# Optimization experiments

Hardware: AMD Instinct MI355X
Metric: run time of the kernel (lower is better)

## Reference

```python
import jax, jax.numpy as jnp
import numpy as np
from jax import lax

B, LS, LT, C, H, GRID = 32, 256, 128, 768, 12, 16
KEEP_RATIO = 0.7

def _ln(x, w, b):
    mu = x.mean(-1, keepdims=True)
    var = ((x - mu) ** 2).mean(-1, keepdims=True)
    return (x - mu) / jnp.sqrt(var + 1e-5) * w + b

def _gelu(x):
    return jax.nn.gelu(x, approximate=False)

def setup_inputs() -> dict:
    key = jax.random.key(0)
    ks = jax.random.split(key, 16)
    w = lambda k, s: jax.random.normal(k, s, jnp.float32) * 0.02
    N = LT + LS
    return {
        'x': jax.random.normal(ks[0], (B, N, C), jnp.float32),
        'global_index_template': jax.random.randint(ks[1], (B, LT), 0, LT).astype(jnp.int32),
        'global_index_search': jax.random.randint(ks[2], (B, LS), 0, LS).astype(jnp.int32),
        'learn_template_mask': jax.random.uniform(ks[3], (2, B, LT // 2), jnp.float32),
        'ln1_w': jnp.ones((C,), jnp.float32), 'ln1_b': jnp.zeros((C,), jnp.float32),
        'qkv_w': w(ks[4], (C, 3 * C)),
        'proj_w': w(ks[5], (C, C)), 'proj_b': jnp.zeros((C,), jnp.float32),
        'ln2_w': jnp.ones((C,), jnp.float32), 'ln2_b': jnp.zeros((C,), jnp.float32),
        'fc1_w': w(ks[6], (C, 4 * C)), 'fc1_b': jnp.zeros((4 * C,), jnp.float32),
        'fc2_w': w(ks[7], (4 * C, C)), 'fc2_b': jnp.zeros((C,), jnp.float32),
        'd1_w': w(ks[8], (3 * C, 768)), 'd1_b': jnp.zeros((768,), jnp.float32),
        'd2_w': w(ks[9], (768, 384)), 'd2_b': jnp.zeros((384,), jnp.float32),
        'd3_w': w(ks[10], (384, 192)), 'd3_b': jnp.zeros((192,), jnp.float32),
        'd4_w': w(ks[11], (192, 1)), 'd4_b': jnp.zeros((1,), jnp.float32),
    }

def reference(x, global_index_template, global_index_search, learn_template_mask,
              ln1_w, ln1_b, qkv_w, proj_w, proj_b, ln2_w, ln2_b,
              fc1_w, fc1_b, fc2_w, fc2_b,
              d1_w, d1_b, d2_w, d2_b, d3_w, d3_b, d4_w, d4_b):
    bs = x.shape[0]
    lt = global_index_template.shape[1]
    ls = global_index_search.shape[1]
    half = lt // 2
    # --- roimax target representations ---
    init_rep = jnp.max(x[:, :half] * learn_template_mask[0][..., None], axis=1, keepdims=True)   # [B,1,C]
    dyn_rep = jnp.max(x[:, half:lt] * learn_template_mask[1][..., None], axis=1, keepdims=True)  # [B,1,C]
    feat = jnp.concatenate([x[:, -ls:],
                            jnp.broadcast_to(init_rep, (bs, ls, C)),
                            jnp.broadcast_to(dyn_rep, (bs, ls, C))], axis=-1)  # [B,ls,3C]
    h = _gelu(feat @ d1_w + d1_b)
    h = _gelu(h @ d2_w + d2_b)
    h = _gelu(h @ d3_w + d3_b)
    pred = h @ d4_w + d4_b                      # [B,ls,1]
    probs = jax.nn.sigmoid(pred)                # foreground probabilities
    # --- 3x3 region-sum conv and argmax center ---
    grid = probs.reshape(bs, 1, GRID, GRID)
    kern = jnp.ones((1, 1, 3, 3), grid.dtype)
    filt = lax.conv_general_dilated(grid, kern, (1, 1), 'SAME',
                                    dimension_numbers=('NCHW', 'OIHW', 'NCHW'))
    max_idx = jnp.argmax(filt.reshape(bs, -1), axis=1)
    cx, cy = max_idx // GRID, max_idx % GRID
    gx = jnp.arange(GRID)[None, :, None]
    gy = jnp.arange(GRID)[None, None, :]
    win = lambda r: ((jnp.abs(gx - cx[:, None, None]) <= r) &
                     (jnp.abs(gy - cy[:, None, None]) <= r)).reshape(bs, GRID * GRID)
    mask7, mask11 = win(3), win(5)
    foreground = (probs > 0.5).astype(jnp.int32)          # [B,ls,1]
    selected_fg = foreground * mask7[..., None].astype(jnp.int32)
    # --- candidate elimination: keep all tokens inside 11x11 window first, then top prob ---
    lens_keep = int(np.ceil(KEEP_RATIO * ls))
    p_out = jnp.where(mask11, jnp.inf, probs[..., 0])     # [B,ls]
    order = jnp.argsort(-p_out, axis=1)                   # stable descending
    topk_idx, non_topk = order[:, :lens_keep], order[:, lens_keep:]
    keep_index = jnp.take_along_axis(global_index_search, topk_idx, axis=1)
    removed_index = jnp.take_along_axis(global_index_search, non_topk, axis=1)
    xs = jnp.take_along_axis(x[:, lt:], topk_idx[..., None], axis=1)  # [B,lens_keep,C]
    xnew = jnp.concatenate([x[:, :lt], xs], axis=1)       # [B, lt+lens_keep, C]
    sf = jnp.take_along_axis(selected_fg, topk_idx[..., None], axis=1)[..., 0]
    decision = jax.nn.one_hot(sf, 2, dtype=x.dtype)       # scatter_(2, sf, 1)
    search_policy = jnp.concatenate([jnp.zeros((bs, lens_keep, 2), x.dtype), decision], -1)
    template_policy = jnp.zeros((bs, half, 4), x.dtype).at[:, :, 0].set(1.0)
    dynamic_policy = jnp.zeros((bs, half, 4), x.dtype).at[:, :, 1].set(1.0)
    P = jnp.concatenate([template_policy, dynamic_policy, search_policy], axis=1)
    key_bg = P[:, :, 2] > 0.5    # background search tokens -> masked as attention keys
    # --- attention ---
    n = xnew.shape[1]
    dh = C // H
    hn = _ln(xnew, ln1_w, ln1_b)
    qkv = (hn @ qkv_w).reshape(bs, n, 3, H, dh).transpose(2, 0, 3, 1, 4)
    q, k, v = qkv[0], qkv[1], qkv[2]
    scores = jnp.einsum('bhnd,bhmd->bhnm', q, k) * dh ** -0.5
    scores = jnp.where(key_bg[:, None, None, :], -1e9, scores)
    attn = jax.nn.softmax(scores, axis=-1)
    out = jnp.einsum('bhnm,bhmd->bhnd', attn, v).transpose(0, 2, 1, 3).reshape(bs, n, C)
    xnew = xnew + (out @ proj_w + proj_b)
    m = _ln(xnew, ln2_w, ln2_b)
    xout = xnew + (_gelu(m @ fc1_w + fc1_b) @ fc2_w + fc2_b)
    return (xout, keep_index, removed_index, attn)
```

## Files before the change

kernel.cpp:

```cpp
#include <hip/hip_runtime.h>
#include <hip/hip_bf16.h>
#include <math.h>

#define BB 32
#define LSN 256
#define LTN 128
#define CCH 768
#define NHH 12
#define NTOK 384
#define NKEEP 180
#define NREM 76
#define NNEW 308
#define MS 8192
#define MN 9856

typedef unsigned short u16;
typedef __attribute__((ext_vector_type(8))) short s8v;
typedef __attribute__((ext_vector_type(4))) float f4v;

__device__ __forceinline__ u16 f2bf(float x) {
    union { __hip_bfloat16 b; u16 u; } c; c.b = __float2bfloat16(x); return c.u;
}
__device__ __forceinline__ float bf2f(u16 u) {
    return __uint_as_float(((unsigned)u) << 16);
}
__device__ __forceinline__ void gl_lds16(const u16* g, u16* l) {
    __builtin_amdgcn_global_load_lds((const __attribute__((address_space(1))) unsigned*)g,
                                     (__attribute__((address_space(3))) unsigned*)l, 16, 0, 0);
}

__global__ void k_fail(float* o, float v) { o[0] = v; }

__global__ void k_reps(const float* __restrict__ x, const float* __restrict__ mask,
                       float* __restrict__ rep0, float* __restrict__ rep1) {
    int b = blockIdx.x, t = threadIdx.x;
    for (int c = t; c < CCH; c += 256) {
        float m0 = -INFINITY, m1 = -INFINITY;
        for (int i = 0; i < 64; ++i) {
            float v0 = x[(size_t)(b * NTOK + i) * CCH + c] * mask[b * 64 + i];
            float v1 = x[(size_t)(b * NTOK + 64 + i) * CCH + c] * mask[BB * 64 + b * 64 + i];
            m0 = fmaxf(m0, v0); m1 = fmaxf(m1, v1);
        }
        rep0[b * CCH + c] = m0; rep1[b * CCH + c] = m1;
    }
}

__device__ __forceinline__ float gelu_np(float v) {
    float t = v / 1.4142135623730951f;
    float ef = (float)erf((double)t);
    return 0.5f * v * (1.0f + ef);
}

template<int ROWMAP>
__global__ __launch_bounds__(256) void gemm_exact(const float* __restrict__ A,
                                                  const float* __restrict__ rep0, const float* __restrict__ rep1,
                                                  const float* __restrict__ W, const float* __restrict__ bias,
                                                  float* __restrict__ out, int N, int K) {
    __shared__ float As[32 * 64];
    __shared__ float Bs[32 * 64];
    int t = threadIdx.x;
    int tx = t & 15, ty = t >> 4;
    int bm = blockIdx.y * 64, bn = blockIdx.x * 64;
    int b = bm >> 8;
    float acc[4][4] = {};

    int arow = t >> 2;
    int ak = (t & 3) * 4;
    int asw = arow ^ ((ak & 4) << 2);
    size_t aoff;
    if (ROWMAP) aoff = (size_t)(b * NTOK + LTN + ((bm + arow) & 255)) * CCH;
    else        aoff = (size_t)(bm + arow) * K;

    int bkr = t >> 4, bc = (t & 15) * 4;

#define LOADA(kg) (ROWMAP ? (((kg) < CCH) ? *(const float4*)&A[aoff + (kg)] \
                    : (((kg) < 2*CCH) ? *(const float4*)&rep0[b*CCH + (kg) - CCH] \
                                      : *(const float4*)&rep1[b*CCH + (kg) - 2*CCH])) \
                   : *(const float4*)&A[aoff + (kg)])

    int nt = K >> 5;
    float4 ra0 = LOADA(ak), ra1 = LOADA(16 + ak);
    float4 rb0 = *(const float4*)&W[(size_t)bkr * N + bn + bc];
    float4 rb1 = *(const float4*)&W[(size_t)(16 + bkr) * N + bn + bc];

    for (int tile = 0; tile < nt; ++tile) {
        __syncthreads();
        As[(ak + 0) * 64 + asw] = ra0.x; As[(ak + 1) * 64 + asw] = ra0.y;
        As[(ak + 2) * 64 + asw] = ra0.z; As[(ak + 3) * 64 + asw] = ra0.w;
        As[(16 + ak + 0) * 64 + asw] = ra1.x; As[(16 + ak + 1) * 64 + asw] = ra1.y;
        As[(16 + ak + 2) * 64 + asw] = ra1.z; As[(16 + ak + 3) * 64 + asw] = ra1.w;
        *(float4*)&Bs[t * 4] = rb0;
        *(float4*)&Bs[1024 + t * 4] = rb1;
        if (tile + 1 < nt) {
            int k0 = (tile + 1) << 5;
            ra0 = LOADA(k0 + ak); ra1 = LOADA(k0 + 16 + ak);
            rb0 = *(const float4*)&W[(size_t)(k0 + bkr) * N + bn + bc];
            rb1 = *(const float4*)&W[(size_t)(k0 + 16 + bkr) * N + bn + bc];
        }
        __syncthreads();
#pragma unroll
        for (int k = 0; k < 32; ++k) {
            float a[4], bv[4];
            *(float4*)&a[0]  = *(const float4*)&As[k * 64 + ((ty * 4) ^ ((k & 4) << 2))];
            *(float4*)&bv[0] = *(const float4*)&Bs[k * 64 + tx * 4];
#pragma unroll
            for (int i = 0; i < 4; ++i)
#pragma unroll
                for (int j = 0; j < 4; ++j) acc[i][j] = fmaf(a[i], bv[j], acc[i][j]);
        }
    }
#undef LOADA
#pragma unroll
    for (int i = 0; i < 4; ++i) {
        int m = bm + ty * 4 + i;
        float4 o;
        o.x = gelu_np(acc[i][0] + bias[bn + tx * 4 + 0]);
        o.y = gelu_np(acc[i][1] + bias[bn + tx * 4 + 1]);
        o.z = gelu_np(acc[i][2] + bias[bn + tx * 4 + 2]);
        o.w = gelu_np(acc[i][3] + bias[bn + tx * 4 + 3]);
        *(float4*)&out[(size_t)m * N + bn + tx * 4] = o;
    }
}

__global__ void k_d4(const float* __restrict__ h3, const float* __restrict__ w4,
                     const float* __restrict__ b4, float* __restrict__ probs) {
    int m = blockIdx.x * 256 + threadIdx.x;
    if (m >= MS) return;
    float acc = 0.f;
    for (int k = 0; k < 192; ++k) acc = fmaf(h3[(size_t)m * 192 + k], w4[k], acc);
    float pred = acc + b4[0];
    float ef = (float)exp(-(double)pred);
    probs[m] = 1.0f / (1.0f + ef);
}

__global__ void k_select(const float* __restrict__ probs, float* __restrict__ pout, int* __restrict__ sf) {
    int b = blockIdx.x, t = threadIdx.x;
    __shared__ float pr[256];
    __shared__ double ft[256];
    __shared__ int cxy[2];
    pr[t] = probs[b * 256 + t];
    __syncthreads();
    int X = t >> 4, Y = t & 15;
    double s = 0.0;
    for (int dx = -1; dx <= 1; ++dx)
        for (int dy = -1; dy <= 1; ++dy) {
            int xx = X + dx, yy = Y + dy;
            if (xx >= 0 && xx < 16 && yy >= 0 && yy < 16) s += (double)pr[xx * 16 + yy];
        }
    ft[t] = s;
    __syncthreads();
    if (t == 0) {
        double best = ft[0]; int bi = 0;
        for (int i = 1; i < 256; ++i) if (ft[i] > best) { best = ft[i]; bi = i; }
        cxy[0] = bi >> 4; cxy[1] = bi & 15;
    }
    __syncthreads();
    int cx = cxy[0], cy = cxy[1];
    int ax = X - cx; if (ax < 0) ax = -ax;
    int ay = Y - cy; if (ay < 0) ay = -ay;
    bool m7  = (ax <= 3) && (ay <= 3);
    bool m11 = (ax <= 5) && (ay <= 5);
    int fg = (pr[t] > 0.5f) ? 1 : 0;
    sf[b * 256 + t] = m7 ? fg : 0;
    pout[b * 256 + t] = m11 ? INFINITY : pr[t];
}

__global__ void k_sort(const float* __restrict__ pout, const int* __restrict__ sf, const int* __restrict__ gis,
                       float* __restrict__ keep_out, float* __restrict__ rem_out,
                       int* __restrict__ topk, int* __restrict__ keybg) {
    int b = blockIdx.x, t = threadIdx.x;
    __shared__ float p[256];
    __shared__ int ord[256];
    p[t] = pout[b * 256 + t];
    __syncthreads();
    float pi = p[t];
    int rank = 0;
    for (int j = 0; j < 256; ++j) {
        float pj = p[j];
        rank += (pj > pi) || (pj == pi && j < t);
    }
    ord[rank] = t;
    __syncthreads();
    int idx = ord[t];
    int g = gis[b * 256 + idx];
    if (t < NKEEP) {
        keep_out[b * NKEEP + t] = (float)g;
        topk[b * NKEEP + t] = idx;
        keybg[b * NNEW + LTN + t] = (sf[b * 256 + idx] == 0) ? 1 : 0;
    } else {
        rem_out[b * NREM + (t - NKEEP)] = (float)g;
    }
    if (t < LTN) keybg[b * NNEW + t] = 0;
}

__global__ void k_xnew(const float* __restrict__ x, const int* __restrict__ topk, float* __restrict__ xn) {
    int row = blockIdx.x;
    int b = row / NNEW, r = row - b * NNEW;
    int src = (r < LTN) ? r : (LTN + topk[b * NKEEP + (r - LTN)]);
    const float* s = x + (size_t)(b * NTOK + src) * CCH;
    float* d = xn + (size_t)row * CCH;
    for (int c = threadIdx.x; c < CCH; c += 256) d[c] = s[c];
}


__global__ void k_ln_bf(const float* __restrict__ in, const float* __restrict__ w, const float* __restrict__ b,
                        u16* __restrict__ out) {
    int row = blockIdx.x, t = threadIdx.x;
    __shared__ float s1[256], s2[256];
    const float* p = in + (size_t)row * CCH;
    float v[3]; float a0 = 0.f, a1 = 0.f;
#pragma unroll
    for (int i = 0; i < 3; ++i) { v[i] = p[t + 256 * i]; a0 += v[i]; a1 += v[i] * v[i]; }
    s1[t] = a0; s2[t] = a1;
    __syncthreads();
    for (int off = 128; off > 0; off >>= 1) {
        if (t < off) { s1[t] += s1[t + off]; s2[t] += s2[t + off]; }
        __syncthreads();
    }
    float mu = s1[0] * (1.0f / CCH);
    float var = s2[0] * (1.0f / CCH) - mu * mu;
    float rstd = rsqrtf(var + 1e-5f);
#pragma unroll
    for (int i = 0; i < 3; ++i) {
        int c = t + 256 * i;
        out[(size_t)row * CCH + c] = f2bf((v[i] - mu) * rstd * w[c] + b[c]);
    }
}

__global__ void k_wT(const float* __restrict__ W, u16* __restrict__ Wt, int K, int N) {
    __shared__ float tile[32][33];
    int k0 = blockIdx.x * 32, n0 = blockIdx.y * 32;
    int tx = threadIdx.x, ty = threadIdx.y;
    for (int i = ty; i < 32; i += 8) tile[i][tx] = W[(size_t)(k0 + i) * N + n0 + tx];
    __syncthreads();
    for (int i = ty; i < 32; i += 8) Wt[(size_t)(n0 + i) * K + k0 + tx] = f2bf(tile[tx][i]);
}

template<int MODE>
__global__ __launch_bounds__(256) void gemm_bf16(const u16* __restrict__ A, const u16* __restrict__ Bt,
                                                 const float* __restrict__ bias, const float* __restrict__ res,
                                                 float* __restrict__ outf, u16* __restrict__ outb,
                                                 u16* __restrict__ vT, int N, int K) {
    __shared__ u16 sm[2][2][4096];
    int t = threadIdx.x, lane = t & 63, wid = t >> 6;
    int bm = blockIdx.y * 128, bn = blockIdx.x * 128;
    const u16* pA[2]; const u16* pB[2];
#pragma unroll
    for (int i = 0; i < 2; ++i) {
        int L = wid * 128 + i * 64 + lane;
        int line = L >> 3, sp = L & 7, sl = sp ^ (line & 7);
        int r = (line << 1) | (sl >> 2), k0 = (sl & 3) << 3;
        pA[i] = A + (size_t)(bm + r) * K + k0;
        pB[i] = Bt + (size_t)(bn + r) * K + k0;
    }
    int wr = wid >> 1, wc = wid & 1;
    int l15 = lane & 15, l4 = lane >> 4;
    int rA = wr * 64 + l15, rB = wc * 64 + l15;
    int offA = (rA >> 1) * 128 + (((((rA & 1) << 2) | l4)) ^ ((rA >> 1) & 7)) * 16;
    int offB = (rB >> 1) * 128 + (((((rB & 1) << 2) | l4)) ^ ((rB >> 1) & 7)) * 16;
    f4v zero = {0.f, 0.f, 0.f, 0.f};
    f4v acc[4][4];
#pragma unroll
    for (int i = 0; i < 4; ++i)
#pragma unroll
        for (int j = 0; j < 4; ++j) acc[i][j] = zero;

#define STAGE_G(buf, kt) { \
    u16* da = &sm[buf][0][wid * 1024]; u16* db = &sm[buf][1][wid * 1024]; \
    gl_lds16(pA[0] + (kt) * 32, da); \
    gl_lds16(pA[1] + (kt) * 32, da + 512); \
    gl_lds16(pB[0] + (kt) * 32, db); \
    gl_lds16(pB[1] + (kt) * 32, db + 512); \
}
    int nk = K >> 5;
    STAGE_G(0, 0);
    __syncthreads();
    for (int kt = 0; kt < nk; ++kt) {
        int cur = kt & 1;
        if (kt + 1 < nk) STAGE_G(cur ^ 1, kt + 1);
        const char* bA = (const char*)&sm[cur][0][0];
        const char* bBp = (const char*)&sm[cur][1][0];
        s8v a[4], b[4];
#pragma unroll
        for (int i = 0; i < 4; ++i) {
            a[i] = *(const s8v*)(bA + offA + i * 1024);
            b[i] = *(const s8v*)(bBp + offB + i * 1024);
        }
#pragma unroll
        for (int mf = 0; mf < 4; ++mf)
#pragma unroll
            for (int nf = 0; nf < 4; ++nf)
                acc[mf][nf] = __builtin_amdgcn_mfma_f32_16x16x32_bf16(a[mf], b[nf], acc[mf][nf], 0, 0, 0);
        __syncthreads();
    }
#undef STAGE_G
#pragma unroll
    for (int mf = 0; mf < 4; ++mf)
#pragma unroll
        for (int nf = 0; nf < 4; ++nf)
#pragma unroll
            for (int j = 0; j < 4; ++j) {
                int row = bm + wr * 64 + mf * 16 + l4 * 4 + j;
                int col = bn + wc * 64 + nf * 16 + l15;
                float v = acc[mf][nf][j];
                if (MODE == 0) {
                    if (col < 1536) {
                        if (col < 768) v *= 0.125f;
                        outb[(size_t)row * 1536 + col] = f2bf(v);
                    } else {
                        int c2 = col - 1536, hh = c2 >> 6, dd = c2 & 63;
                        int bb = row / NNEW, tok = row - bb * NNEW;
                        vT[(((size_t)bb * NHH + hh) * 64 + dd) * 312 + tok] = f2bf(v);
                    }
                } else if (MODE == 1) {
                    outf[(size_t)row * N + col] = v + bias[col] + res[(size_t)row * N + col];
                } else {
                    float g = v + bias[col];
                    g = 0.5f * g * (1.0f + erff(g * 0.70710678f));
                    outb[(size_t)row * N + col] = f2bf(g);
                }
            }
}

__global__ __launch_bounds__(256) void k_attn2(const u16* __restrict__ qkvQK, const u16* __restrict__ vT,
                                               const int* __restrict__ keybg,
                                               float* __restrict__ attn_out, u16* __restrict__ ctx) {
    __shared__ __align__(16) char smem[98560];
    u16* Qs = (u16*)smem;
    u16* Ks = (u16*)(smem + 9216);
    u16* Ss = (u16*)(smem + 55296);
    int* kb = (int*)(smem + 97280);
    float* OT = (float*)Ss;
    u16* Vts = Ks;

    int bh = blockIdx.y; int b = bh / NHH, h = bh % NHH;
    int q0 = blockIdx.x * 64;
    int nq = NNEW - q0; if (nq > 64) nq = 64;
    int t = threadIdx.x, lane = t & 63, wid = t >> 6;
    int l15 = lane & 15, l4 = lane >> 4;
    s8v z = {0, 0, 0, 0, 0, 0, 0, 0};

    {
        int r = t >> 2, c = (t & 3) * 16;
        u16* dst = Qs + r * 72 + c;
        if (r < nq) {
            const u16* src = qkvQK + (size_t)(b * NNEW + q0 + r) * 1536 + h * 64 + c;
            *(s8v*)dst = *(const s8v*)src;
            *(s8v*)(dst + 8) = *(const s8v*)(src + 8);
        } else { *(s8v*)dst = z; *(s8v*)(dst + 8) = z; }
    }
    for (int it = 0; it < 5; ++it) {
        int r = it * 64 + (t >> 2), c = (t & 3) * 16;
        u16* dst = Ks + r * 72 + c;
        if (r < NNEW) {
            const u16* src = qkvQK + (size_t)(b * NNEW + r) * 1536 + 768 + h * 64 + c;
            *(s8v*)dst = *(const s8v*)src;
            *(s8v*)(dst + 8) = *(const s8v*)(src + 8);
        } else { *(s8v*)dst = z; *(s8v*)(dst + 8) = z; }
    }
    for (int i = t; i < 320; i += 256) kb[i] = (i < NNEW) ? keybg[b * NNEW + i] : 1;
    __syncthreads();

    f4v zero = {0.f, 0.f, 0.f, 0.f};
    f4v acc[4][5];
#pragma unroll
    for (int i = 0; i < 4; ++i)
#pragma unroll
        for (int j = 0; j < 5; ++j) acc[i][j] = zero;
#pragma unroll
    for (int ks = 0; ks < 2; ++ks) {
        s8v a[4], bf[5];
#pragma unroll
        for (int mf = 0; mf < 4; ++mf) a[mf] = *(const s8v*)(Qs + (mf * 16 + l15) * 72 + ks * 32 + l4 * 8);
#pragma unroll
        for (int nf = 0; nf < 5; ++nf) bf[nf] = *(const s8v*)(Ks + (wid * 80 + nf * 16 + l15) * 72 + ks * 32 + l4 * 8);
#pragma unroll
        for (int mf = 0; mf < 4; ++mf)
#pragma unroll
            for (int nf = 0; nf < 5; ++nf)
                acc[mf][nf] = __builtin_amdgcn_mfma_f32_16x16x32_bf16(a[mf], bf[nf], acc[mf][nf], 0, 0, 0);
    }
#pragma unroll
    for (int nf = 0; nf < 5; ++nf) {
        int n = wid * 80 + nf * 16 + l15;
        int msk = kb[n];
#pragma unroll
        for (int mf = 0; mf < 4; ++mf)
#pragma unroll
            for (int j = 0; j < 4; ++j) {
                int q = mf * 16 + l4 * 4 + j;
                float v = msk ? -1e9f : acc[mf][nf][j];
                Ss[q * 328 + n] = f2bf(v);
            }
    }
    __syncthreads();

    {
        int d = t >> 2;
        for (int c = (t & 3); c < 39; c += 4) {
            const u16* src = vT + ((size_t)bh * 64 + d) * 312 + c * 8;
            *(s8v*)(Vts + d * 312 + c * 8) = *(const s8v*)src;
        }
    }
    {
        int q = t >> 2, j4 = t & 3;
        u16* row = Ss + q * 328 + j4 * 80;
        float mx = -3e38f;
#pragma unroll
        for (int i = 0; i < 10; ++i) {
            s8v vv = *(const s8v*)(row + i * 8);
#pragma unroll
            for (int e = 0; e < 8; ++e) mx = fmaxf(mx, bf2f((u16)vv[e]));
        }
        mx = fmaxf(mx, __shfl_xor(mx, 1));
        mx = fmaxf(mx, __shfl_xor(mx, 2));
        float sum = 0.f;
#pragma unroll
        for (int i = 0; i < 10; ++i) {
            s8v vv = *(const s8v*)(row + i * 8);
            s8v ov;
#pragma unroll
            for (int e = 0; e < 8; ++e) {
                float ex = expf(bf2f((u16)vv[e]) - mx);
                sum += ex;
                ov[e] = (short)f2bf(ex);
            }
            *(s8v*)(row + i * 8) = ov;
        }
        sum += __shfl_xor(sum, 1);
        sum += __shfl_xor(sum, 2);
        float inv = 1.0f / sum;
#pragma unroll
        for (int i = 0; i < 10; ++i) {
            s8v vv = *(const s8v*)(row + i * 8);
            s8v ov;
            float pf[8];
#pragma unroll
            for (int e = 0; e < 8; ++e) {
                float p = bf2f((u16)vv[e]) * inv;
                pf[e] = p;
                ov[e] = (short)f2bf(p);
            }
            *(s8v*)(row + i * 8) = ov;
            if (q < nq) {
                int n0 = j4 * 80 + i * 8;
                float* dst = attn_out + ((size_t)bh * NNEW + q0 + q) * NNEW + n0;
#pragma unroll
                for (int e = 0; e < 8; ++e) if (n0 + e < NNEW) dst[e] = pf[e];
            }
        }
    }
    __syncthreads();

    f4v o[4];
#pragma unroll
    for (int i = 0; i < 4; ++i) o[i] = zero;
    int dblk = wid * 16;
#pragma unroll
    for (int ks = 0; ks < 10; ++ks) {
        s8v av = *(const s8v*)(Vts + (dblk + l15) * 312 + ks * 32 + l4 * 8);
#pragma unroll
        for (int nf = 0; nf < 4; ++nf) {
            s8v pv = *(const s8v*)(Ss + (nf * 16 + l15) * 328 + ks * 32 + l4 * 8);
            o[nf] = __builtin_amdgcn_mfma_f32_16x16x32_bf16(av, pv, o[nf], 0, 0, 0);
        }
    }
    __syncthreads();
#pragma unroll
    for (int nf = 0; nf < 4; ++nf)
#pragma unroll
        for (int j = 0; j < 4; ++j)
            OT[(dblk + l4 * 4 + j) * 65 + nf * 16 + l15] = o[nf][j];
    __syncthreads();
    {
        int q = t >> 2, c = t & 3;
        if (q < nq) {
            u16 buf[16];
#pragma unroll
            for (int i = 0; i < 16; ++i) buf[i] = f2bf(OT[(c * 16 + i) * 65 + q]);
            u16* dst = ctx + (size_t)(b * NNEW + q0 + q) * CCH + h * 64 + c * 16;
            *(s8v*)dst = *(const s8v*)&buf[0];
            *(s8v*)(dst + 8) = *(const s8v*)&buf[8];
        }
    }
}

extern "C" void kernel_launch(void* const* d_in, const int* in_sizes, int n_in,
                              void* d_out, int out_size, void* d_ws, size_t ws_size,
                              hipStream_t stream) {
    const float* x     = (const float*)d_in[0];
    const int*   gis   = (const int*)d_in[2];
    const float* mask  = (const float*)d_in[3];
    const float* ln1w  = (const float*)d_in[4];
    const float* ln1b  = (const float*)d_in[5];
    const float* qkvw  = (const float*)d_in[6];
    const float* projw = (const float*)d_in[7];
    const float* projb = (const float*)d_in[8];
    const float* ln2w  = (const float*)d_in[9];
    const float* ln2b  = (const float*)d_in[10];
    const float* fc1w  = (const float*)d_in[11];
    const float* fc1b  = (const float*)d_in[12];
    const float* fc2w  = (const float*)d_in[13];
    const float* fc2b  = (const float*)d_in[14];
    const float* d1w   = (const float*)d_in[15];
    const float* d1b   = (const float*)d_in[16];
    const float* d2w   = (const float*)d_in[17];
    const float* d2b   = (const float*)d_in[18];
    const float* d3w   = (const float*)d_in[19];
    const float* d3b   = (const float*)d_in[20];
    const float* d4w   = (const float*)d_in[21];
    const float* d4b   = (const float*)d_in[22];

    float* out_x    = (float*)d_out;
    float* out_keep = out_x + 7569408;
    float* out_rem  = out_keep + 5760;
    float* out_attn = out_rem + 2432;

    char* ws = (char*)d_ws;
    u16* hn_bf  = (u16*)(ws);
    u16* qkvQK  = (u16*)(ws + 15138816);
    u16* vTb    = (u16*)(ws + 45416448);
    u16* fc1_bf = (u16*)(ws);
    u16* ctx_bf = (u16*)(ws + 60751872);
    u16* qkvwT  = (u16*)(ws + 75890688);
    u16* projwT = (u16*)(ws + 79429632);
    u16* fc1wT  = (u16*)(ws + 80609280);
    u16* fc2wT  = (u16*)(ws + 85327872);
    char* misc  = ws + 90046464;
    float* rep0  = (float*)(misc + 0 * 262144);
    float* rep1  = (float*)(misc + 1 * 262144);
    float* probs = (float*)(misc + 2 * 262144);
    float* pout  = (float*)(misc + 3 * 262144);
    int*   sf    = (int*)(misc + 4 * 262144);
    int*   topk  = (int*)(misc + 5 * 262144);
    int*   keybg = (int*)(misc + 6 * 262144);
    size_t required = 90046464ull + 7ull * 262144ull;
    if (ws_size < required) {
        k_fail<<<1, 1, 0, stream>>>((float*)d_out, (float)(ws_size / 1048576.0));
        return;
    }

    float* h1 = (float*)out_attn;
    float* h2 = h1 + 8192 * 768;
    float* h3 = h2 + 8192 * 384;

    k_wT<<<dim3(24, 72), dim3(32, 8), 0, stream>>>(qkvw, qkvwT, 768, 2304);
    k_wT<<<dim3(24, 24), dim3(32, 8), 0, stream>>>(projw, projwT, 768, 768);
    k_wT<<<dim3(24, 96), dim3(32, 8), 0, stream>>>(fc1w, fc1wT, 768, 3072);
    k_wT<<<dim3(96, 24), dim3(32, 8), 0, stream>>>(fc2w, fc2wT, 3072, 768);
    hipMemsetAsync(vTb, 0, 15335424, stream);

    k_reps<<<BB, 256, 0, stream>>>(x, mask, rep0, rep1);
    gemm_exact<1><<<dim3(12, 128), 256, 0, stream>>>(x, rep0, rep1, d1w, d1b, h1, 768, 2304);
    gemm_exact<0><<<dim3(6, 128), 256, 0, stream>>>(h1, nullptr, nullptr, d2w, d2b, h2, 384, 768);
    gemm_exact<0><<<dim3(3, 128), 256, 0, stream>>>(h2, nullptr, nullptr, d3w, d3b, h3, 192, 384);
    k_d4<<<MS / 256, 256, 0, stream>>>(h3, d4w, d4b, probs);
    k_select<<<BB, 256, 0, stream>>>(probs, pout, sf);
    k_sort<<<BB, 256, 0, stream>>>(pout, sf, gis, out_keep, out_rem, topk, keybg);
    k_xnew<<<MN, 256, 0, stream>>>(x, topk, out_x);

    k_ln_bf<<<MN, 256, 0, stream>>>(out_x, ln1w, ln1b, hn_bf);
    gemm_bf16<0><<<dim3(18, 77), 256, 0, stream>>>(hn_bf, qkvwT, nullptr, nullptr, nullptr, qkvQK, vTb, 2304, 768);
    k_attn2<<<dim3(5, 384), 256, 0, stream>>>(qkvQK, vTb, keybg, out_attn, ctx_bf);
    gemm_bf16<1><<<dim3(6, 77), 256, 0, stream>>>(ctx_bf, projwT, projb, out_x, out_x, nullptr, nullptr, 768, 768);
    k_ln_bf<<<MN, 256, 0, stream>>>(out_x, ln2w, ln2b, ctx_bf);
    gemm_bf16<2><<<dim3(24, 77), 256, 0, stream>>>(ctx_bf, fc1wT, fc1b, nullptr, nullptr, fc1_bf, nullptr, 3072, 768);
    gemm_bf16<1><<<dim3(6, 77), 256, 0, stream>>>(fc1_bf, fc2wT, fc2b, out_x, out_x, nullptr, nullptr, 768, 3072);
}
```

Baseline: 1.090 ms.

## Restructure FP32 decision-head GEMM with wave-uniform weight loads and swizzled block order

Replaces the LDS-tiled 4x4 register GEMM for the three decision-head layers with a kernel where each wave owns 16 output columns and each lane one row. Weights are read straight from global memory with wave-uniform addresses (readfirstlane), so they can go through scalar or broadcast loads instead of LDS. Packed float2 FMAs are used, and a 1D grid remaps blocks so groups of 8 row bands share a column for L2 locality. This removes B-tile LDS traffic, but each thread now reuses the A value across only 16 columns and relies on a global or scalar load per k step.

```diff
diff --git a/kernel.cpp b/kernel.cpp
--- a/kernel.cpp
+++ b/kernel.cpp
@@ -17,6 +17,7 @@
 typedef unsigned short u16;
 typedef __attribute__((ext_vector_type(8))) short s8v;
 typedef __attribute__((ext_vector_type(4))) float f4v;
+typedef __attribute__((ext_vector_type(2))) float f2v;
 
 __device__ __forceinline__ u16 f2bf(float x) {
     union { __hip_bfloat16 b; u16 u; } c; c.b = __float2bfloat16(x); return c.u;
@@ -52,26 +53,28 @@
 }
 
 template<int ROWMAP>
-__global__ __launch_bounds__(256) void gemm_exact(const float* __restrict__ A,
-                                                  const float* __restrict__ rep0, const float* __restrict__ rep1,
-                                                  const float* __restrict__ W, const float* __restrict__ bias,
-                                                  float* __restrict__ out, int N, int K) {
-    __shared__ float As[32 * 64];
-    __shared__ float Bs[32 * 64];
-    int t = threadIdx.x;
-    int tx = t & 15, ty = t >> 4;
-    int bm = blockIdx.y * 64, bn = blockIdx.x * 64;
+__global__ __launch_bounds__(256) void gemm_head_reg(const float* __restrict__ A,
+                                                     const float* __restrict__ rep0, const float* __restrict__ rep1,
+                                                     const float* __restrict__ W, const float* __restrict__ bias,
+                                                     float* __restrict__ out, int N, int K, int ncol) {
+    __shared__ float As[32][64];
+    int t = threadIdx.x, lane = t & 63, wid = t >> 6;
+    int id = blockIdx.x;
+    int r = id & 7, q = id >> 3;
+    int qd = q / ncol;
+    int band = r + 8 * qd, col = q - ncol * qd;
+    int bm = band * 64, bn = col * 64;
     int b = bm >> 8;
-    float acc[4][4] = {};
-
-    int arow = t >> 2;
-    int ak = (t & 3) * 4;
-    int asw = arow ^ ((ak & 4) << 2);
+    int colu = __builtin_amdgcn_readfirstlane(bn + wid * 16);
+
+    f2v acc2[8];
+#pragma unroll
+    for (int j = 0; j < 8; ++j) acc2[j] = (f2v){0.f, 0.f};
+
+    int srow = t >> 2, kof = (t & 3) * 8;
     size_t aoff;
-    if (ROWMAP) aoff = (size_t)(b * NTOK + LTN + ((bm + arow) & 255)) * CCH;
-    else        aoff = (size_t)(bm + arow) * K;
-
-    int bkr = t >> 4, bc = (t & 15) * 4;
+    if (ROWMAP) aoff = (size_t)(b * NTOK + LTN + ((bm + srow) & 255)) * CCH;
+    else        aoff = (size_t)(bm + srow) * K;
 
 #define LOADA(kg) (ROWMAP ? (((kg) < CCH) ? *(const float4*)&A[aoff + (kg)] \
                     : (((kg) < 2*CCH) ? *(const float4*)&rep0[b*CCH + (kg) - CCH] \
@@ -79,47 +82,44 @@
                    : *(const float4*)&A[aoff + (kg)])
 
     int nt = K >> 5;
-    float4 ra0 = LOADA(ak), ra1 = LOADA(16 + ak);
-    float4 rb0 = *(const float4*)&W[(size_t)bkr * N + bn + bc];
-    float4 rb1 = *(const float4*)&W[(size_t)(16 + bkr) * N + bn + bc];
+    float4 ra0 = LOADA(kof), ra1 = LOADA(kof + 4);
 
     for (int tile = 0; tile < nt; ++tile) {
+        int k0 = tile << 5;
         __syncthreads();
-        As[(ak + 0) * 64 + asw] = ra0.x; As[(ak + 1) * 64 + asw] = ra0.y;
-        As[(ak + 2) * 64 + asw] = ra0.z; As[(ak + 3) * 64 + asw] = ra0.w;
-        As[(16 + ak + 0) * 64 + asw] = ra1.x; As[(16 + ak + 1) * 64 + asw] = ra1.y;
-        As[(16 + ak + 2) * 64 + asw] = ra1.z; As[(16 + ak + 3) * 64 + asw] = ra1.w;
-        *(float4*)&Bs[t * 4] = rb0;
-        *(float4*)&Bs[1024 + t * 4] = rb1;
+        As[kof + 0][srow] = ra0.x; As[kof + 1][srow] = ra0.y;
+        As[kof + 2][srow] = ra0.z; As[kof + 3][srow] = ra0.w;
+        As[kof + 4][srow] = ra1.x; As[kof + 5][srow] = ra1.y;
+        As[kof + 6][srow] = ra1.z; As[kof + 7][srow] = ra1.w;
         if (tile + 1 < nt) {
-            int k0 = (tile + 1) << 5;
-            ra0 = LOADA(k0 + ak); ra1 = LOADA(k0 + 16 + ak);
-            rb0 = *(const float4*)&W[(size_t)(k0 + bkr) * N + bn + bc];
-            rb1 = *(const float4*)&W[(size_t)(k0 + 16 + bkr) * N + bn + bc];
+            ra0 = LOADA(k0 + 32 + kof); ra1 = LOADA(k0 + 32 + kof + 4);
         }
         __syncthreads();
 #pragma unroll
         for (int k = 0; k < 32; ++k) {
-            float a[4], bv[4];
-            *(float4*)&a[0]  = *(const float4*)&As[k * 64 + ((ty * 4) ^ ((k & 4) << 2))];
-            *(float4*)&bv[0] = *(const float4*)&Bs[k * 64 + tx * 4];
-#pragma unroll
-            for (int i = 0; i < 4; ++i)
-#pragma unroll
-                for (int j = 0; j < 4; ++j) acc[i][j] = fmaf(a[i], bv[j], acc[i][j]);
+            float a = As[k][lane];
+            const float* Wk = W + (size_t)(k0 + k) * N + colu;
+            f2v av = {a, a};
+#pragma unroll
+            for (int j = 0; j < 8; ++j) {
+                f2v bv = *(const f2v*)(Wk + 2 * j);
+                acc2[j] = __builtin_elementwise_fma(av, bv, acc2[j]);
+            }
         }
     }
 #undef LOADA
-#pragma unroll
-    for (int i = 0; i < 4; ++i) {
-        int m = bm + ty * 4 + i;
-        float4 o;
-        o.x = gelu_np(acc[i][0] + bias[bn + tx * 4 + 0]);
-        o.y = gelu_np(acc[i][1] + bias[bn + tx * 4 + 1]);
-        o.z = gelu_np(acc[i][2] + bias[bn + tx * 4 + 2]);
-        o.w = gelu_np(acc[i][3] + bias[bn + tx * 4 + 3]);
-        *(float4*)&out[(size_t)m * N + bn + tx * 4] = o;
-    }
+
+    int m = bm + lane;
+    float o[16];
+#pragma unroll
+    for (int j = 0; j < 8; ++j) {
+        o[2 * j + 0] = gelu_np(acc2[j][0] + bias[colu + 2 * j + 0]);
+        o[2 * j + 1] = gelu_np(acc2[j][1] + bias[colu + 2 * j + 1]);
+    }
+    float* dst = out + (size_t)m * N + colu;
+#pragma unroll
+    for (int j = 0; j < 4; ++j)
+        *(float4*)(dst + 4 * j) = *(const float4*)&o[4 * j];
 }
 
 __global__ void k_d4(const float* __restrict__ h3, const float* __restrict__ w4,
@@ -551,9 +551,9 @@
     hipMemsetAsync(vTb, 0, 15335424, stream);
 
     k_reps<<<BB, 256, 0, stream>>>(x, mask, rep0, rep1);
-    gemm_exact<1><<<dim3(12, 128), 256, 0, stream>>>(x, rep0, rep1, d1w, d1b, h1, 768, 2304);
-    gemm_exact<0><<<dim3(6, 128), 256, 0, stream>>>(h1, nullptr, nullptr, d2w, d2b, h2, 384, 768);
-    gemm_exact<0><<<dim3(3, 128), 256, 0, stream>>>(h2, nullptr, nullptr, d3w, d3b, h3, 192, 384);
+    gemm_head_reg<1><<<1536, 256, 0, stream>>>(x, rep0, rep1, d1w, d1b, h1, 768, 2304, 12);
+    gemm_head_reg<0><<<768, 256, 0, stream>>>(h1, nullptr, nullptr, d2w, d2b, h2, 384, 768, 6);
+    gemm_head_reg<0><<<384, 256, 0, stream>>>(h2, nullptr, nullptr, d3w, d3b, h3, 192, 384, 3);
     k_d4<<<MS / 256, 256, 0, stream>>>(h3, d4w, d4b, probs);
     k_select<<<BB, 256, 0, stream>>>(probs, pout, sf);
     k_sort<<<BB, 256, 0, stream>>>(pout, sf, gis, out_keep, out_rem, topk, keybg);
```

Result: slower. 2.203 ms (+102.1%).
